# Kernel tuning notes

Hardware: AMD Instinct MI355X
Metric: run time of the kernel (lower is better)

Reference implementation:

```python
import jax, jax.numpy as jnp
import numpy as np

N = 100000   # nodes
E = 3200000  # directed edges
F = 16       # num_features (colors)


def setup_inputs() -> dict:
    key = jax.random.key(0)
    ks = jax.random.split(key, 5)
    x = jax.random.normal(ks[0], (N, F), dtype=jnp.float32)
    edge_index = jax.random.randint(ks[1], (2, E), 0, N)
    # Glorot-ish scaled weights for the 5 identical blocks (F->64->32->F)
    W1 = jax.random.normal(ks[2], (5, F, 64), dtype=jnp.float32) * (1.0 / np.sqrt(F))
    W2 = jax.random.normal(ks[3], (5, 64, 32), dtype=jnp.float32) * (1.0 / np.sqrt(64))
    W3 = jax.random.normal(ks[4], (5, 32, F), dtype=jnp.float32) * (1.0 / np.sqrt(32))
    b1 = jnp.zeros((5, 64), dtype=jnp.float32)
    b2 = jnp.zeros((5, 32), dtype=jnp.float32)
    b3 = jnp.zeros((5, F), dtype=jnp.float32)
    return {"x": x, "edge_index": edge_index,
            "W1": W1, "b1": b1, "W2": W2, "b2": b2, "W3": W3, "b3": b3}


def _gcn(x, W, b, src, dst, norm, n):
    # GCNConv: project, then symmetric-normalized neighbor sum (self-loops in src/dst)
    h = x @ W                                   # [n, d_out]
    msg = h[src] * norm[:, None]                # [e+n, d_out] gather + scale
    out = jax.ops.segment_sum(msg, dst, num_segments=n)
    return out + b


def reference(x, edge_index, W1, b1, W2, b2, W3, b3):
    n = x.shape[0]
    loops = jnp.arange(n)
    src = jnp.concatenate([edge_index[0], loops])  # add self loops (PyG default)
    dst = jnp.concatenate([edge_index[1], loops])
    deg = jax.ops.segment_sum(jnp.ones(src.shape[0], jnp.float32), dst, num_segments=n)
    dis = jax.lax.rsqrt(jnp.maximum(deg, 1.0))     # deg >= 1 due to self loops
    norm = dis[src] * dis[dst]
    for i in range(5):
        x = jax.nn.relu(_gcn(x, W1[i], b1[i], src, dst, norm, n))
        x = jax.nn.relu(_gcn(x, W2[i], b2[i], src, dst, norm, n))
        x = jax.nn.softmax(_gcn(x, W3[i], b3[i], src, dst, norm, n), axis=1)
    return x
```

## Files before the change

kernel.cpp:

```cpp
#include <hip/hip_runtime.h>

#define NN 100000
#define NE 3200000
#define SLAB 80
#define SLAB4 (SLAB / 4)
#define NB 196
#define BSH 9
#define BCAP 20480
#define NBB 500
#define EPB 6400
#define CAP 64

typedef int      vi4 __attribute__((ext_vector_type(4)));
typedef float    vf4 __attribute__((ext_vector_type(4)));
typedef _Float16 vh8 __attribute__((ext_vector_type(8)));

#if __has_builtin(__builtin_amdgcn_global_load_lds)
#define HAS_GLL 1
typedef const __attribute__((address_space(1))) void* gas1_t;
typedef __attribute__((address_space(3))) void* las3_t;
#define GLL4(g, l)  __builtin_amdgcn_global_load_lds((gas1_t)(g), (las3_t)(l), 4, 0, 0)
#define GLL16(g, l) __builtin_amdgcn_global_load_lds((gas1_t)(g), (las3_t)(l), 16, 0, 0)
#else
#define HAS_GLL 0
#endif

__device__ inline void wave_sync_lds() {
    asm volatile("s_waitcnt lgkmcnt(0)" ::: "memory");
    __builtin_amdgcn_sched_barrier(0);
}


__global__ __launch_bounds__(512)
void k_bucket(const int* __restrict__ src, const int* __restrict__ dst,
              int* __restrict__ gcur, int* __restrict__ entries) {
    __shared__ int stage[NB * CAP];
    __shared__ int sfill[NB];
    __shared__ int sbase[NB];
    int tid = threadIdx.x;
    for (int i = tid; i < NB; i += 512) sfill[i] = 0;
    __syncthreads();

    int e0 = blockIdx.x * EPB;
    const vi4* d4 = (const vi4*)(dst + e0);
    const vi4* s4 = (const vi4*)(src + e0);
    for (int i = tid; i < EPB / 4; i += 512) {
        vi4 dv = __builtin_nontemporal_load(d4 + i);
        vi4 sv = __builtin_nontemporal_load(s4 + i);
        #pragma unroll
        for (int j = 0; j < 4; j++) {
            int d = dv[j];
            int b = d >> BSH;
            int v = sv[j] | ((d & 511) << 17);
            int p = atomicAdd(&sfill[b], 1);
            if (p < CAP) {
                stage[b * CAP + p] = v;
            } else {
                int gp = atomicAdd(&gcur[b], 1);
                if (gp < BCAP) entries[b * BCAP + gp] = v;
            }
        }
    }
    __syncthreads();

    if (tid < NB) {
        int cnt = min(sfill[tid], CAP);
        sbase[tid] = atomicAdd(&gcur[tid], cnt);
    }
    __syncthreads();

    int wid = tid >> 6, lane = tid & 63;
    for (int b = wid; b < NB; b += 8) {
        int cnt = min(sfill[b], CAP);
        int gbase = sbase[b];
        for (int j = lane; j < cnt; j += 64) {
            int pos = gbase + j;
            if (pos < BCAP)
                __builtin_nontemporal_store(stage[b * CAP + j], entries + b * BCAP + pos);
        }
    }
}

__global__ __launch_bounds__(512)
void k_csr(const int* __restrict__ gcur, const int* __restrict__ entries,
           int* __restrict__ col, int* __restrict__ cnt4, float* __restrict__ dis,
           const float* __restrict__ x, vh8* __restrict__ xs8,
           vh8* __restrict__ h3s8, vh8* __restrict__ h2s8) {
    __shared__ int lcur[512];
    int tid = threadIdx.x;
    int b = blockIdx.x;
    lcur[tid] = 0;
    __syncthreads();
    int nE = min(gcur[b], BCAP);
    const int* ep = entries + b * BCAP;
    int nbase = b << BSH;
    for (int e = tid; e < nE; e += 512) {
        int v = __builtin_nontemporal_load(ep + e);
        int s = v & 0x1FFFF;
        int local = v >> 17;
        int p = atomicAdd(&lcur[local], 1);
        if (p < SLAB) col[(size_t)(nbase + local) * SLAB + p] = s;
    }
    __syncthreads();
    {
        int node = nbase + tid;
        if (node < NN) {
            int c = lcur[tid];
            float dn = rsqrtf((float)(c + 1));
            dis[node] = dn;
            int cc = min(c, SLAB);
            int c4 = (cc + 3) >> 2;
            cnt4[node] = c4;
            int* slab = col + (size_t)node * SLAB;
            for (int k = cc; k < c4 * 4; k++) slab[k] = NN;
            const vf4* xr = (const vf4*)(x + (size_t)node * 16);
            vh8 o0, o1;
            #pragma unroll
            for (int i = 0; i < 4; i++) {
                o0[i]     = (_Float16)(xr[0][i] * dn);
                o0[i + 4] = (_Float16)(xr[1][i] * dn);
                o1[i]     = (_Float16)(xr[2][i] * dn);
                o1[i + 4] = (_Float16)(xr[3][i] * dn);
            }
            xs8[(size_t)node * 2 + 0] = o0;
            xs8[(size_t)node * 2 + 1] = o1;
        }
    }
    if (b == 0 && tid < 8) {
        vh8 z = {(_Float16)0.f, (_Float16)0.f, (_Float16)0.f, (_Float16)0.f,
                 (_Float16)0.f, (_Float16)0.f, (_Float16)0.f, (_Float16)0.f};
        if (tid < 2)      xs8[NN * 2 + tid] = z;
        else if (tid < 4) h3s8[NN * 2 + (tid - 2)] = z;
        else              h2s8[NN * 4 + (tid - 4)] = z;
    }
}

template<int CH, int UNROLL>
__device__ inline void gather4w(const vh8* __restrict__ in, const int4* __restrict__ cp,
                                int c4, int node, int d, int h, float* acc) {
    vh8 self = in[node * CH + d];
    #pragma unroll
    for (int i = 0; i < 8; i++) acc[i] = h ? 0.f : (float)self[i];
    #pragma unroll UNROLL
    for (int k = h; k < c4; k += 4) {
        vi4 cs = __builtin_nontemporal_load((const vi4*)(cp + k));
        vh8 a = in[cs.x * CH + d];
        vh8 b = in[cs.y * CH + d];
        vh8 c = in[cs.z * CH + d];
        vh8 e = in[cs.w * CH + d];
        #pragma unroll
        for (int i = 0; i < 8; i++)
            acc[i] += ((float)a[i] + (float)b[i]) + ((float)c[i] + (float)e[i]);
    }
    #pragma unroll
    for (int i = 0; i < 8; i++) acc[i] += __shfl_xor(acc[i], 1);
    #pragma unroll
    for (int i = 0; i < 8; i++) acc[i] += __shfl_xor(acc[i], 2);
}


__global__ __launch_bounds__(256)
void k_layerA(const vh8* __restrict__ xs, const int* __restrict__ cnt4,
              const int4* __restrict__ colv, const float* __restrict__ dis,
              const float* __restrict__ W1, const float* __restrict__ b1,
              const float* __restrict__ W2, _Float16* __restrict__ h2s) {
    __shared__ float sW1[16 * 64];
    __shared__ float sW2[64 * 32];
    __shared__ float sb1[64];
    __shared__ float st[32 * 16];
    __shared__ float sx1[32 * 68];
    int tid = threadIdx.x;
    int wid = tid >> 6, lane = tid & 63;

#if HAS_GLL
    GLL16(W1 + wid * 256 + lane * 4, sW1 + wid * 256);
    GLL16(W2 + (wid * 2 + 0) * 256 + lane * 4, sW2 + (wid * 2 + 0) * 256);
    GLL16(W2 + (wid * 2 + 1) * 256 + lane * 4, sW2 + (wid * 2 + 1) * 256);
    if (wid == 0) GLL4(b1 + lane, sb1);
#endif

    int nl = tid >> 3, ll = tid & 7, d = ll >> 2, h = ll & 3;
    int node = blockIdx.x * 32 + nl;
    float dn = dis[node];
    float acc[8];
    gather4w<2, 2>(xs, colv + (size_t)node * SLAB4, cnt4[node], node, d, h, acc);

#if !HAS_GLL
    {
        ((vf4*)sW1)[tid] = ((const vf4*)W1)[tid];
        ((vf4*)sW2)[tid] = ((const vf4*)W2)[tid];
        ((vf4*)sW2)[tid + 256] = ((const vf4*)W2)[tid + 256];
        if (tid < 64) sb1[tid] = b1[tid];
    }
#endif

    if (h == 0) {
        vf4 v0 = {acc[0] * dn, acc[1] * dn, acc[2] * dn, acc[3] * dn};
        vf4 v1 = {acc[4] * dn, acc[5] * dn, acc[6] * dn, acc[7] * dn};
        ((vf4*)st)[nl * 4 + d * 2 + 0] = v0;
        ((vf4*)st)[nl * 4 + d * 2 + 1] = v1;
    }
    __syncthreads();

    int c = tid & 63, g = tid >> 6;
    #pragma unroll
    for (int p = 0; p < 2; p++) {
        int nb = g * 8 + p * 4;
        float a0 = sb1[c], a1 = a0, a2 = a0, a3 = a0;
        #pragma unroll
        for (int kq = 0; kq < 4; kq++) {
            vf4 s0 = *(const vf4*)(st + (nb + 0) * 16 + kq * 4);
            vf4 s1 = *(const vf4*)(st + (nb + 1) * 16 + kq * 4);
            vf4 s2 = *(const vf4*)(st + (nb + 2) * 16 + kq * 4);
            vf4 s3 = *(const vf4*)(st + (nb + 3) * 16 + kq * 4);
            #pragma unroll
            for (int i = 0; i < 4; i++) {
                float w = sW1[(kq * 4 + i) * 64 + c];
                a0 += s0[i] * w; a1 += s1[i] * w; a2 += s2[i] * w; a3 += s3[i] * w;
            }
        }
        sx1[(nb + 0) * 68 + c] = fmaxf(a0, 0.f);
        sx1[(nb + 1) * 68 + c] = fmaxf(a1, 0.f);
        sx1[(nb + 2) * 68 + c] = fmaxf(a2, 0.f);
        sx1[(nb + 3) * 68 + c] = fmaxf(a3, 0.f);
    }
    wave_sync_lds();

    int c2 = tid & 31, g2 = tid >> 5;
    const float* x0 = sx1 + (g2 * 4 + 0) * 68;
    const float* x1r = sx1 + (g2 * 4 + 1) * 68;
    const float* x2r = sx1 + (g2 * 4 + 2) * 68;
    const float* x3r = sx1 + (g2 * 4 + 3) * 68;
    float a0 = 0.f, a1 = 0.f, a2 = 0.f, a3 = 0.f;
    #pragma unroll
    for (int kq = 0; kq < 16; kq++) {
        vf4 xa = *(const vf4*)(x0 + kq * 4);
        vf4 xb = *(const vf4*)(x1r + kq * 4);
        vf4 xc = *(const vf4*)(x2r + kq * 4);
        vf4 xd = *(const vf4*)(x3r + kq * 4);
        #pragma unroll
        for (int i = 0; i < 4; i++) {
            float w = sW2[(kq * 4 + i) * 32 + c2];
            a0 += xa[i] * w; a1 += xb[i] * w; a2 += xc[i] * w; a3 += xd[i] * w;
        }
    }
    {
        int gn = blockIdx.x * 32 + g2 * 4;
        h2s[(size_t)(gn + 0) * 32 + c2] = (_Float16)(a0 * dis[gn + 0]);
        h2s[(size_t)(gn + 1) * 32 + c2] = (_Float16)(a1 * dis[gn + 1]);
        h2s[(size_t)(gn + 2) * 32 + c2] = (_Float16)(a2 * dis[gn + 2]);
        h2s[(size_t)(gn + 3) * 32 + c2] = (_Float16)(a3 * dis[gn + 3]);
    }
}

__global__ __launch_bounds__(256)
void k_aggmm3(const vh8* __restrict__ h2s, const int* __restrict__ cnt4,
              const int4* __restrict__ colv, const float* __restrict__ dis,
              const float* __restrict__ b2, const float* __restrict__ W3,
              _Float16* __restrict__ h3s) {
    __shared__ float sW[32 * 16];
    __shared__ float st[16 * 40];
    int tid = threadIdx.x;
    int wid = tid >> 6, lane = tid & 63;

#if HAS_GLL
    if (wid < 2) GLL16(W3 + wid * 256 + lane * 4, sW + wid * 256);
#endif

    int nl = tid >> 4, ll = tid & 15, d = ll >> 2, h = ll & 3;
    int node = blockIdx.x * 16 + nl;
    float dn = dis[node];
    float acc[8];
    gather4w<4, 2>(h2s, colv + (size_t)node * SLAB4, cnt4[node], node, d, h, acc);

#if !HAS_GLL
    sW[tid] = W3[tid];
    sW[tid + 256] = W3[tid + 256];
#endif

    if (h == 0) {
        vf4 bl = ((const vf4*)b2)[d * 2];
        vf4 bh = ((const vf4*)b2)[d * 2 + 1];
        vf4 v0, v1;
        #pragma unroll
        for (int i = 0; i < 4; i++) {
            v0[i] = fmaxf(acc[i] * dn + bl[i], 0.f);
            v1[i] = fmaxf(acc[i + 4] * dn + bh[i], 0.f);
        }
        vf4* sp = (vf4*)(st + nl * 40 + d * 8);
        sp[0] = v0;
        sp[1] = v1;
    }
    __syncthreads();

    int c = tid & 15, n = tid >> 4;
    float a0 = 0.f;
    #pragma unroll
    for (int kq = 0; kq < 8; kq++) {
        vf4 s = *(const vf4*)(st + n * 40 + kq * 4);
        #pragma unroll
        for (int i = 0; i < 4; i++)
            a0 += s[i] * sW[(kq * 4 + i) * 16 + c];
    }
    int gn = blockIdx.x * 16 + n;
    h3s[(size_t)gn * 16 + c] = (_Float16)(a0 * dis[gn]);
}

__global__ __launch_bounds__(256)
void k_agg_soft(const vh8* __restrict__ in, const int* __restrict__ cnt4,
                const int4* __restrict__ colv, const float* __restrict__ dis,
                const float* __restrict__ bias, float* __restrict__ out,
                vh8* __restrict__ out2, int last) {
    int tid = threadIdx.x;
    int nl = tid >> 3, ll = tid & 7, d = ll >> 2, h = ll & 3;
    int node = blockIdx.x * 32 + nl;
    float dn = dis[node];
    float acc[8];
    gather4w<2, 2>(in, colv + (size_t)node * SLAB4, cnt4[node], node, d, h, acc);
    vf4 bl = ((const vf4*)bias)[d * 2];
    vf4 bh = ((const vf4*)bias)[d * 2 + 1];
    #pragma unroll
    for (int i = 0; i < 4; i++) { acc[i] = acc[i] * dn + bl[i]; acc[i + 4] = acc[i + 4] * dn + bh[i]; }
    float m = acc[0];
    #pragma unroll
    for (int i = 1; i < 8; i++) m = fmaxf(m, acc[i]);
    m = fmaxf(m, __shfl_xor(m, 4));
    float ev[8], s = 0.f;
    #pragma unroll
    for (int i = 0; i < 8; i++) { ev[i] = __expf(acc[i] - m); s += ev[i]; }
    s += __shfl_xor(s, 4);
    float inv = 1.0f / s;
    if (h == 0) {
        if (last) {
            vf4 o0 = {ev[0] * inv, ev[1] * inv, ev[2] * inv, ev[3] * inv};
            vf4 o1 = {ev[4] * inv, ev[5] * inv, ev[6] * inv, ev[7] * inv};
            __builtin_nontemporal_store(o0, (vf4*)out + (size_t)node * 4 + d * 2);
            __builtin_nontemporal_store(o1, (vf4*)out + (size_t)node * 4 + d * 2 + 1);
        }
        vh8 ho;
        #pragma unroll
        for (int i = 0; i < 8; i++) ho[i] = (_Float16)(ev[i] * inv * dn);
        out2[(size_t)node * 2 + d] = ho;
    }
}


static inline size_t align_up(size_t v, size_t a) { return (v + a - 1) & ~(a - 1); }

extern "C" void kernel_launch(void* const* d_in, const int* in_sizes, int n_in,
                              void* d_out, int out_size, void* d_ws, size_t ws_size,
                              hipStream_t stream) {
    const float* x   = (const float*)d_in[0];
    const int*   ei  = (const int*)d_in[1];
    const float* W1  = (const float*)d_in[2];
    const float* b1  = (const float*)d_in[3];
    const float* W2  = (const float*)d_in[4];
    const float* b2  = (const float*)d_in[5];
    const float* W3  = (const float*)d_in[6];
    const float* b3  = (const float*)d_in[7];
    float* outp = (float*)d_out;

    const int* src = ei;
    const int* dst = ei + NE;

    char* ws = (char*)d_ws;
    size_t off = 0;
    auto carve = [&](size_t bytes) { void* p = ws + off; off = align_up(off + bytes, 256); return p; };
    int*      gcur  = (int*)     carve(NB * 4);
    int*      cnt4  = (int*)     carve(NN * 4);
    float*    dis   = (float*)   carve(NN * 4);
    int*      col   = (int*)     carve((size_t)NN * SLAB * 4);
    _Float16* xs    = (_Float16*)carve((size_t)(NN + 1) * 16 * 2);
    _Float16* h3s   = (_Float16*)carve((size_t)(NN + 1) * 16 * 2);
    int*      entries = (int*)   carve((size_t)NB * BCAP * 4);
    _Float16* h2s   = (_Float16*)carve((size_t)(NN + 1) * 32 * 2);
    (void)ws_size; (void)n_in; (void)in_sizes; (void)out_size;

    hipMemsetAsync(gcur, 0, NB * 4, stream);
    k_bucket<<<NBB, 512, 0, stream>>>(src, dst, gcur, entries);
    k_csr<<<NB, 512, 0, stream>>>(gcur, entries, col, cnt4, dis, x,
                                  (vh8*)xs, (vh8*)h3s, (vh8*)h2s);

    const int gA = NN / 32;
    const int gB = NN / 16;
    const int gC = NN / 32;

    for (int l = 0; l < 5; l++) {
        k_layerA<<<gA, 256, 0, stream>>>((const vh8*)xs, cnt4, (const int4*)col, dis,
                                         W1 + l * 16 * 64, b1 + l * 64, W2 + l * 64 * 32, h2s);
        k_aggmm3<<<gB, 256, 0, stream>>>((const vh8*)h2s, cnt4, (const int4*)col, dis,
                                         b2 + l * 32, W3 + l * 32 * 16, h3s);
        k_agg_soft<<<gC, 256, 0, stream>>>((const vh8*)h3s, cnt4, (const int4*)col, dis,
                                           b3 + l * 16, outp, (vh8*)xs, l == 4 ? 1 : 0);
    }
}
```

Measured before the change: 598.1 us.

## Split each destination bucket into four source-range sub-buckets for CSR build

Result: slower. 708.9 us (+18.5%).

```diff
diff --git a/kernel.cpp b/kernel.cpp
--- a/kernel.cpp
+++ b/kernel.cpp
@@ -6,10 +6,10 @@
 #define SLAB4 (SLAB / 4)
 #define NB 196
 #define BSH 9
-#define BCAP 20480
 #define NBB 500
 #define EPB 6400
 #define CAP 64
+#define BCAPQ 5120
 
 typedef int      vi4 __attribute__((ext_vector_type(4)));
 typedef float    vf4 __attribute__((ext_vector_type(4)));
@@ -30,13 +30,16 @@
     __builtin_amdgcn_sched_barrier(0);
 }
 
+__device__ inline int src_region(int s) {
+    return (s >= 25000) + (s >= 50000) + (s >= 75000);
+}
+
 
 __global__ __launch_bounds__(512)
 void k_bucket(const int* __restrict__ src, const int* __restrict__ dst,
-              int* __restrict__ gcur, int* __restrict__ entries) {
+              int* __restrict__ gcur4, int* __restrict__ entries4) {
     __shared__ int stage[NB * CAP];
     __shared__ int sfill[NB];
-    __shared__ int sbase[NB];
     int tid = threadIdx.x;
     for (int i = tid; i < NB; i += 512) sfill[i] = 0;
     __syncthreads();
@@ -56,33 +59,47 @@
             if (p < CAP) {
                 stage[b * CAP + p] = v;
             } else {
-                int gp = atomicAdd(&gcur[b], 1);
-                if (gp < BCAP) entries[b * BCAP + gp] = v;
+                int r = src_region(sv[j]);
+                int gp = atomicAdd(&gcur4[b * 4 + r], 1);
+                if (gp < BCAPQ) entries4[((size_t)b * 4 + r) * BCAPQ + gp] = v;
             }
         }
     }
     __syncthreads();
 
-    if (tid < NB) {
-        int cnt = min(sfill[tid], CAP);
-        sbase[tid] = atomicAdd(&gcur[tid], cnt);
-    }
-    __syncthreads();
-
     int wid = tid >> 6, lane = tid & 63;
+    unsigned long long lmask = (1ull << lane) - 1;
     for (int b = wid; b < NB; b += 8) {
         int cnt = min(sfill[b], CAP);
-        int gbase = sbase[b];
-        for (int j = lane; j < cnt; j += 64) {
-            int pos = gbase + j;
-            if (pos < BCAP)
-                __builtin_nontemporal_store(stage[b * CAP + j], entries + b * BCAP + pos);
+        int v = 0, r = -1;
+        if (lane < cnt) {
+            v = stage[b * CAP + lane];
+            r = src_region(v & 0x1FFFF);
+        }
+        unsigned long long m0 = __ballot(r == 0);
+        unsigned long long m1 = __ballot(r == 1);
+        unsigned long long m2 = __ballot(r == 2);
+        unsigned long long m3 = __ballot(r == 3);
+        int myn = 0;
+        if (lane == 0) myn = (int)__popcll(m0);
+        else if (lane == 1) myn = (int)__popcll(m1);
+        else if (lane == 2) myn = (int)__popcll(m2);
+        else if (lane == 3) myn = (int)__popcll(m3);
+        int mybase = (lane < 4) ? atomicAdd(&gcur4[b * 4 + lane], myn) : 0;
+        int base0 = __shfl(mybase, 0), base1 = __shfl(mybase, 1);
+        int base2 = __shfl(mybase, 2), base3 = __shfl(mybase, 3);
+        if (r >= 0) {
+            unsigned long long m = (r == 0) ? m0 : (r == 1) ? m1 : (r == 2) ? m2 : m3;
+            int base = (r == 0) ? base0 : (r == 1) ? base1 : (r == 2) ? base2 : base3;
+            int pos = base + (int)__popcll(m & lmask);
+            if (pos < BCAPQ)
+                __builtin_nontemporal_store(v, entries4 + ((size_t)b * 4 + r) * BCAPQ + pos);
         }
     }
 }
 
 __global__ __launch_bounds__(512)
-void k_csr(const int* __restrict__ gcur, const int* __restrict__ entries,
+void k_csr(const int* __restrict__ gcur4, const int* __restrict__ entries4,
            int* __restrict__ col, int* __restrict__ cnt4, float* __restrict__ dis,
            const float* __restrict__ x, vh8* __restrict__ xs8,
            vh8* __restrict__ h3s8, vh8* __restrict__ h2s8) {
@@ -91,17 +108,20 @@
     int b = blockIdx.x;
     lcur[tid] = 0;
     __syncthreads();
-    int nE = min(gcur[b], BCAP);
-    const int* ep = entries + b * BCAP;
     int nbase = b << BSH;
-    for (int e = tid; e < nE; e += 512) {
-        int v = __builtin_nontemporal_load(ep + e);
-        int s = v & 0x1FFFF;
-        int local = v >> 17;
-        int p = atomicAdd(&lcur[local], 1);
-        if (p < SLAB) col[(size_t)(nbase + local) * SLAB + p] = s;
-    }
-    __syncthreads();
+    #pragma unroll
+    for (int q = 0; q < 4; q++) {
+        int nE = min(gcur4[b * 4 + q], BCAPQ);
+        const int* eq = entries4 + ((size_t)b * 4 + q) * BCAPQ;
+        for (int e = tid; e < nE; e += 512) {
+            int v = __builtin_nontemporal_load(eq + e);
+            int s = v & 0x1FFFF;
+            int local = v >> 17;
+            int p = atomicAdd(&lcur[local], 1);
+            if (p < SLAB) col[(size_t)(nbase + local) * SLAB + p] = s;
+        }
+        __syncthreads();
+    }
     {
         int node = nbase + tid;
         if (node < NN) {
@@ -366,19 +386,19 @@
     char* ws = (char*)d_ws;
     size_t off = 0;
     auto carve = [&](size_t bytes) { void* p = ws + off; off = align_up(off + bytes, 256); return p; };
-    int*      gcur  = (int*)     carve(NB * 4);
+    int*      gcur4 = (int*)     carve(NB * 4 * 4);
     int*      cnt4  = (int*)     carve(NN * 4);
     float*    dis   = (float*)   carve(NN * 4);
     int*      col   = (int*)     carve((size_t)NN * SLAB * 4);
     _Float16* xs    = (_Float16*)carve((size_t)(NN + 1) * 16 * 2);
     _Float16* h3s   = (_Float16*)carve((size_t)(NN + 1) * 16 * 2);
-    int*      entries = (int*)   carve((size_t)NB * BCAP * 4);
+    int*      entries4 = (int*)  carve((size_t)NB * 4 * BCAPQ * 4);
     _Float16* h2s   = (_Float16*)carve((size_t)(NN + 1) * 32 * 2);
     (void)ws_size; (void)n_in; (void)in_sizes; (void)out_size;
 
-    hipMemsetAsync(gcur, 0, NB * 4, stream);
-    k_bucket<<<NBB, 512, 0, stream>>>(src, dst, gcur, entries);
-    k_csr<<<NB, 512, 0, stream>>>(gcur, entries, col, cnt4, dis, x,
+    hipMemsetAsync(gcur4, 0, NB * 4 * 4, stream);
+    k_bucket<<<NBB, 512, 0, stream>>>(src, dst, gcur4, entries4);
+    k_csr<<<NB, 512, 0, stream>>>(gcur4, entries4, col, cnt4, dis, x,
                                   (vh8*)xs, (vh8*)h3s, (vh8*)h2s);
 
     const int gA = NN / 32;
```
